# Kernel optimization log

Measured on AMD Instinct MI355X. Metric: run time of the kernel, lower is better.

Reference implementation:

```python
import jax, jax.numpy as jnp
import numpy as np

B, C_ENC, H, W = 8, 512, 96, 96
N_SAMP = 64            # num_samples in forward
N_NODES = 2 * N_SAMP   # 64 pos + 64 neg per image
D = 256                # node feature dim after head_in_ln
N_HEADS = 8
DH = D // N_HEADS
SINKHORN_ITERS = 10


def _ln(x):
    # LayerNorm(elementwise_affine=False)
    m = x.mean(-1, keepdims=True)
    v = x.var(-1, keepdims=True)
    return (x - m) / jnp.sqrt(v + 1e-5)


def setup_inputs() -> dict:
    key = jax.random.key(0)
    ks = jax.random.split(key, 12)
    std = 0.01  # matches nn.init.normal_(std=0.01) in _init_weights
    inp = {
        "feat_s": jax.random.normal(ks[0], (B, C_ENC, H, W), jnp.float32),
        "score_s": jax.random.normal(ks[1], (B, 1, H, W), jnp.float32),
        "feat_t": jax.random.normal(ks[2], (B, C_ENC, H, W), jnp.float32),
        "score_t": jax.random.normal(ks[3], (B, 1, H, W), jnp.float32),
        "head_W1": std * jax.random.normal(ks[4], (C_ENC, D), jnp.float32),
        "head_b1": jnp.zeros((D,), jnp.float32),
        "head_W2": std * jax.random.normal(ks[5], (D, D), jnp.float32),
        "head_b2": jnp.zeros((D,), jnp.float32),
        "intra_W": jax.random.normal(ks[6], (4, D, D), jnp.float32) / jnp.sqrt(jnp.float32(D)),
        "intra_b": jnp.zeros((4, D), jnp.float32),
        "cross_W": jax.random.normal(ks[7], (4, D, D), jnp.float32) / jnp.sqrt(jnp.float32(D)),
        "cross_b": jnp.zeros((4, D), jnp.float32),
        "cls_W1": std * jax.random.normal(ks[8], (D, 128), jnp.float32),
        "cls_b1": jnp.zeros((128,), jnp.float32),
        "cls_W2": std * jax.random.normal(ks[9], (128, 1), jnp.float32),
        "cls_b2": jnp.zeros((1,), jnp.float32),
        "aff_A": jax.random.normal(ks[10], (D, D), jnp.float32) / jnp.sqrt(jnp.float32(D)),
    }
    return inp


def _sample_points(feat, score):
    # torch version: boolean-mask nonzero + random gather of 64 pos / 64 neg spatial
    # locations per image. JIT-friendly deterministic equivalent: top-64 highest
    # sigmoid scores = positives, top-64 lowest = negatives.
    s = jax.nn.sigmoid(score[:, 0].reshape(B, -1))            # [B, H*W]
    _, pos_idx = jax.lax.top_k(s, N_SAMP)
    _, neg_idx = jax.lax.top_k(-s, N_SAMP)
    idx = jnp.concatenate([pos_idx, neg_idx], axis=1)         # [B, 128]
    ff = feat.reshape(B, C_ENC, -1)                           # [B, 512, H*W]
    nodes = jnp.take_along_axis(ff, idx[:, None, :], axis=2)  # [B, 512, 128]
    nodes = nodes.transpose(0, 2, 1)                          # [B, 128, 512]
    labels = jnp.concatenate(
        [jnp.ones((B, N_SAMP, 1), feat.dtype), jnp.zeros((B, N_SAMP, 1), feat.dtype)], axis=1)
    return nodes, labels


def _mha(xq, xkv, Wp, bp):
    # standard multi-head attention (MultiHeadAttentionWrapper)
    q = xq @ Wp[0] + bp[0]
    k = xkv @ Wp[1] + bp[1]
    v = xkv @ Wp[2] + bp[2]
    sh = lambda t: t.reshape(t.shape[0], t.shape[1], N_HEADS, DH)
    att = jnp.einsum("bqhd,bkhd->bhqk", sh(q), sh(k)) / jnp.sqrt(jnp.float32(DH))
    att = jax.nn.softmax(att, axis=-1)
    o = jnp.einsum("bhqk,bkhd->bqhd", att, sh(v)).reshape(xq.shape[0], xq.shape[1], D)
    return o @ Wp[3] + bp[3], att.mean(1)


def _forward(feat_s, score_s, feat_t, score_t, head_W1, head_b1, head_W2, head_b2,
             intra_W, intra_b, cross_W, cross_b, cls_W1, cls_b1, cls_W2, cls_b2, aff_A):
    n1, l1 = _sample_points(feat_s, score_s)
    n2, l2 = _sample_points(feat_t, score_t)

    # head_in_ln: Linear -> LN -> ReLU -> Linear -> LN
    head = lambda x: _ln(jax.nn.relu(_ln(x @ head_W1 + head_b1)) @ head_W2 + head_b2)
    n1, n2 = head(n1), head(n2)

    # intra-domain graph (self-attention), shared weights for both domains
    n1, _ = _mha(n1, n1, intra_W, intra_b)
    n2, _ = _mha(n2, n2, intra_W, intra_b)

    # cross-domain graph (cross-attention both directions, shared weights)
    c1, _ = _mha(n1, n2, cross_W, cross_b)
    c2, _ = _mha(n2, n1, cross_W, cross_b)
    n1, n2 = c1, c2

    # node classification loss (BCEWithLogits, mean)
    cls = lambda x: jax.nn.relu(x @ cls_W1 + cls_b1) @ cls_W2 + cls_b2
    def bce_logits(logit, lab):
        return jnp.mean(jnp.maximum(logit, 0) - logit * lab + jnp.log1p(jnp.exp(-jnp.abs(logit))))
    node_loss = bce_logits(cls(n1), l1) + bce_logits(cls(n2), l2)

    # affinity + InstanceNorm2d(1) + sinkhorn refine
    Mmat = jnp.einsum("bnd,de,bme->bnm", n1, aff_A, n2)       # [B, 128, 128]
    mu = Mmat.mean((1, 2), keepdims=True)
    var = Mmat.var((1, 2), keepdims=True)
    K = (Mmat - mu) / jnp.sqrt(var + 1e-5)
    for _ in range(SINKHORN_ITERS):  # log-space row/col normalization
        K = K - jax.nn.logsumexp(K, axis=2, keepdims=True)
        K = K - jax.nn.logsumexp(K, axis=1, keepdims=True)
    P = jnp.exp(K)

    # matching loss = BCEFocalLoss(gamma=2, alpha=0.25) vs label-agreement matrix
    gt = (l1[:, :, 0][:, :, None] == l2[:, :, 0][:, None, :]).astype(P.dtype)
    pt = jnp.clip(P, 1e-6, 1.0 - 1e-6)
    mat_loss = jnp.mean(-0.25 * (1 - pt) ** 2 * gt * jnp.log(pt)
                        - 0.75 * pt ** 2 * (1 - gt) * jnp.log(1 - pt))

    total_loss = node_loss + 10.0 * mat_loss
    return n1, total_loss


def reference(feat_s, score_s, feat_t, score_t, head_W1, head_b1, head_W2, head_b2,
              intra_W, intra_b, cross_W, cross_b, cls_W1, cls_b1, cls_W2, cls_b2, aff_A):
    return _forward(feat_s, score_s, feat_t, score_t, head_W1, head_b1, head_W2, head_b2,
                    intra_W, intra_b, cross_W, cross_b, cls_W1, cls_b1, cls_W2, cls_b2, aff_A)
```

## Files before the change

kernel.cpp:

```cpp
#include <hip/hip_runtime.h>
#include <math.h>

#define BIMG 8
#define HW 9216
#define CENC 512
#define NN 128
#define DD 256
#define NHEAD 8
#define DH 32
#define ROWS1 1024
#define ROWS2 2048
#define TAILB 520

typedef unsigned long long ull;
typedef unsigned short u16;
typedef __attribute__((ext_vector_type(4))) float f32x4;
typedef __attribute__((ext_vector_type(4))) unsigned u32x4;
typedef __attribute__((ext_vector_type(2))) unsigned u32x2;

__device__ __forceinline__ u16 f2bf(float f) {
  unsigned u = __float_as_uint(f);
  u += 0x7fffu + ((u >> 16) & 1u);
  return (u16)(u >> 16);
}
__device__ __forceinline__ float bf2f(unsigned h) { return __uint_as_float(h << 16); }
__device__ __forceinline__ unsigned pack2(float a, float b) {
  return (unsigned)f2bf(a) | ((unsigned)f2bf(b) << 16);
}
__device__ __forceinline__ void mfma_b(f32x4& acc, u32x4 a, u32x4 b) {
  asm volatile("v_mfma_f32_16x16x32_bf16 %0, %1, %2, %0" : "+v"(acc) : "v"(a), "v"(b));
}
__device__ __forceinline__ void mfma_s(f32x4& acc, u32x4 a, u32x4 b) {
  asm volatile("s_nop 1\n\tv_mfma_f32_16x16x32_bf16 %0, %1, %2, %0" : "+v"(acc) : "v"(a), "v"(b));
}

__device__ __forceinline__ ull cmpex_keep(ull k, ull o, bool keepMax) {
  return ((k > o) == keepMax) ? k : o;
}
__device__ __forceinline__ void bsort64(ull& k, int lane) {
#pragma unroll
  for (int size = 2; size <= 64; size <<= 1) {
#pragma unroll
    for (int stride = size >> 1; stride > 0; stride >>= 1) {
      ull o = __shfl_xor(k, stride);
      bool keepMax = (((lane & size) == 0) == ((lane & stride) == 0));
      k = cmpex_keep(k, o, keepMax);
    }
  }
}
__device__ __forceinline__ void bmerge64(ull& top, ull b, int lane) {
  ull rev = __shfl_xor(b, 63);
  ull m = top > rev ? top : rev;
#pragma unroll
  for (int stride = 32; stride > 0; stride >>= 1) {
    ull o = __shfl_xor(m, stride);
    m = cmpex_keep(m, o, (lane & stride) == 0);
  }
  top = m;
}
__device__ __forceinline__ ull lds_merge(ull a, ull brev, int lane) {
  ull m = a > brev ? a : brev;
#pragma unroll
  for (int stride = 32; stride > 0; stride >>= 1) {
    ull o = __shfl_xor(m, stride);
    m = cmpex_keep(m, o, (lane & stride) == 0);
  }
  return m;
}

__global__ __launch_bounds__(512) void head_kernel(const float* __restrict__ score_s,
                                                   const float* __restrict__ score_t,
                                                   int* __restrict__ idx_out,
                                                   float* __restrict__ loss_acc,
                                                   const float* __restrict__ hw1,
                                                   const float* __restrict__ hw2,
                                                   const float* __restrict__ iw,
                                                   const float* __restrict__ cw,
                                                   const float* __restrict__ aw,
                                                   const float* __restrict__ clsW1,
                                                   const float* __restrict__ intra_b,
                                                   const float* __restrict__ cross_b,
                                                   u16* __restrict__ wt,
                                                   u16* __restrict__ w1t,
                                                   u16* __restrict__ wt_f,
                                                   float* __restrict__ bfq) {
  __shared__ union {
    struct { ull sm[512]; float tile[32][33]; } a;
    struct { float Wo[32][264]; float Wc[256][40]; } b;
  } HS;
  int tid = threadIdx.x;
  if (blockIdx.x < 32) {
    int blk = blockIdx.x;
    int bi = blk >> 1, neg = blk & 1;
    int lane = tid & 63, w = tid >> 6;
    if (blk == 0 && tid < 4) loss_acc[tid] = 0.f;
    const float* sp = (bi < 8 ? score_s : score_t) + (size_t)(bi & 7) * HW;
    int q0 = w * 18;
    ull keys[18];
#pragma unroll
    for (int j = 0; j < 18; ++j) {
      float x = sp[(q0 + j) * 64 + lane];
      unsigned ub = __float_as_uint(x);
      unsigned u = (ub & 0x80000000u) ? ~ub : (ub | 0x80000000u);
      if (neg) u = ~u;
      int gi = (q0 + j) * 64 + lane;
      keys[j] = ((ull)u << 32) | (unsigned)(~gi);
    }
    ull top1 = keys[0]; bsort64(top1, lane);
    ull top2 = keys[9]; bsort64(top2, lane);
#pragma unroll
    for (int j = 1; j < 9; ++j) {
      ull k1 = keys[j], k2 = keys[9 + j];
      bsort64(k1, lane);
      bsort64(k2, lane);
      bmerge64(top1, k1, lane);
      bmerge64(top2, k2, lane);
    }
    bmerge64(top1, top2, lane);
    HS.a.sm[w * 64 + lane] = top1;
    __syncthreads();
    if (w < 4) {
      ull m = lds_merge(HS.a.sm[(2 * w) * 64 + lane],
                        HS.a.sm[(2 * w + 1) * 64 + (63 - lane)], lane);
      HS.a.sm[(2 * w) * 64 + lane] = m;
    }
    __syncthreads();
    if (w < 2) {
      ull m = lds_merge(HS.a.sm[(4 * w) * 64 + lane],
                        HS.a.sm[(4 * w + 2) * 64 + (63 - lane)], lane);
      HS.a.sm[(4 * w) * 64 + lane] = m;
    }
    __syncthreads();
    if (w == 0) {
      ull m = lds_merge(HS.a.sm[lane], HS.a.sm[4 * 64 + (63 - lane)], lane);
      idx_out[bi * NN + neg * 64 + lane] = (int)(~(unsigned)(m & 0xffffffffull));
    }
  } else if (blockIdx.x < 800) {
    int bid = blockIdx.x - 32;
    const float* src; u16* dst; int K, k0, n0;
    if (bid < 128) {
      src = hw1; dst = wt; K = 512;
      k0 = (bid >> 3) * 32; n0 = (bid & 7) * 32;
    } else {
      int id2 = bid - 128;
      int m = id2 >> 6, tt = id2 & 63;
      K = 256;
      k0 = (tt >> 3) * 32; n0 = (tt & 7) * 32;
      src = (m == 0) ? hw2 : (m < 5) ? iw + (size_t)(m - 1) * 65536
          : (m < 9) ? cw + (size_t)(m - 5) * 65536 : aw;
      dst = wt + 131072 + (size_t)m * 65536;
    }
    int r = tid >> 3, c = (tid & 7) * 4;
    if (tid < 256) {
      float4 v = *(const float4*)&src[(size_t)(k0 + r) * 256 + n0 + c];
      HS.a.tile[r][c] = v.x; HS.a.tile[r][c + 1] = v.y;
      HS.a.tile[r][c + 2] = v.z; HS.a.tile[r][c + 3] = v.w;
    }
    __syncthreads();
    if (tid < 256) {
      u32x2 o;
      o[0] = pack2(HS.a.tile[c][r], HS.a.tile[c + 1][r]);
      o[1] = pack2(HS.a.tile[c + 2][r], HS.a.tile[c + 3][r]);
      *(u32x2*)&dst[(size_t)(n0 + r) * K + k0 + c] = o;
    }
  } else if (blockIdx.x < 832) {
    int bid3 = blockIdx.x - 800;
    int k0 = (bid3 >> 2) * 32, n0 = (bid3 & 3) * 32;
    int r = tid >> 3, c = (tid & 7) * 4;
    if (tid < 256) {
      float4 v = *(const float4*)&clsW1[(size_t)(k0 + r) * 128 + n0 + c];
      HS.a.tile[r][c] = v.x; HS.a.tile[r][c + 1] = v.y;
      HS.a.tile[r][c + 2] = v.z; HS.a.tile[r][c + 3] = v.w;
    }
    __syncthreads();
    if (tid < 256) {
      u32x2 o;
      o[0] = pack2(HS.a.tile[c][r], HS.a.tile[c + 1][r]);
      o[1] = pack2(HS.a.tile[c + 2][r], HS.a.tile[c + 3][r]);
      *(u32x2*)&w1t[(size_t)(n0 + r) * 256 + k0 + c] = o;
    }
  } else {
    int bid4 = blockIdx.x - 832;
    int z = bid4 >> 6, tt = bid4 & 63;
    int k0 = (tt >> 3) * 32, n0 = (tt & 7) * 32;
    const float* Wo = iw + 3 * 65536;
    const float* Wc = cw + (size_t)z * 65536;
    for (int e = tid; e < 2048; e += 512) {
      int row = e >> 6, c4 = (e & 63) * 4;
      *(float4*)&HS.b.Wo[row][c4] = *(const float4*)&Wo[(size_t)(k0 + row) * 256 + c4];
    }
    for (int e = tid; e < 2048; e += 512) {
      int row = e >> 3, c4 = (e & 7) * 4;
      *(float4*)&HS.b.Wc[row][c4] = *(const float4*)&Wc[(size_t)row * 256 + n0 + c4];
    }
    __syncthreads();
    int k = tid >> 4, half = (tid >> 3) & 1, nb = (tid & 7) * 4;
    float a0 = 0.f, a1 = 0.f, a2 = 0.f, a3 = 0.f;
    int jb = half * 128;
#pragma unroll 8
    for (int j = 0; j < 128; ++j) {
      float wo = HS.b.Wo[k][jb + j];
      float4 wc = *(const float4*)&HS.b.Wc[jb + j][nb];
      a0 += wo * wc.x; a1 += wo * wc.y; a2 += wo * wc.z; a3 += wo * wc.w;
    }
    a0 += __shfl_xor(a0, 8); a1 += __shfl_xor(a1, 8);
    a2 += __shfl_xor(a2, 8); a3 += __shfl_xor(a3, 8);
    if (half == 0) {
      u16* dst = wt_f + (size_t)z * 65536;
      dst[(size_t)(n0 + nb + 0) * 256 + k0 + k] = f2bf(a0);
      dst[(size_t)(n0 + nb + 1) * 256 + k0 + k] = f2bf(a1);
      dst[(size_t)(n0 + nb + 2) * 256 + k0 + k] = f2bf(a2);
      dst[(size_t)(n0 + nb + 3) * 256 + k0 + k] = f2bf(a3);
    }
    if (k0 == 0 && tid < 32) {
      float b = 0.f;
      const float* bo = intra_b + 768;
      for (int j = 0; j < 256; ++j) b += bo[j] * HS.b.Wc[j][tid];
      bfq[z * 256 + n0 + tid] = b + cross_b[z * 256 + n0 + tid];
    }
  }
}

__global__ __launch_bounds__(512) void gemm1_fused(const float* __restrict__ feat_s,
                                                   const float* __restrict__ feat_t,
                                                   const int* __restrict__ idxb,
                                                   const u16* __restrict__ wt_h1,
                                                   const float* __restrict__ head_b1,
                                                   u16* __restrict__ bufA,
                                                   float* __restrict__ st1) {
  __shared__ u16 As[16][520];
  __shared__ u16 Bs[256][40];
  int t = threadIdx.x, l = t & 63, w = t >> 6;
  int m0 = blockIdx.x * 16;
#pragma unroll
  for (int row = 0; row < 16; ++row) {
    int grow = m0 + row;
    int bi = grow >> 7, n = grow & 127, b = bi & 7;
    const float* fp = (bi < 8) ? feat_s : feat_t;
    int pos = idxb[bi * NN + n];
    As[row][t] = f2bf(fp[(size_t)b * CENC * HW + (size_t)t * HW + pos]);
  }
  __syncthreads();
  f32x4 acc[2];
  acc[0] = (f32x4){0.f, 0.f, 0.f, 0.f};
  acc[1] = (f32x4){0.f, 0.f, 0.f, 0.f};
  for (int kc = 0; kc < 16; ++kc) {
#pragma unroll
    for (int i = 0; i < 2; ++i) {
      int e = t + i * 512;
      int nn2 = e >> 2, ch8 = (e & 3) * 8;
      *(u32x4*)&Bs[nn2][ch8] = *(const u32x4*)&wt_h1[(size_t)nn2 * 512 + kc * 32 + ch8];
    }
    __syncthreads();
    u32x4 af = *(const u32x4*)&As[l & 15][kc * 32 + (l >> 4) * 8];
#pragma unroll
    for (int i = 0; i < 2; ++i) {
      u32x4 bf = *(const u32x4*)&Bs[w * 32 + i * 16 + (l & 15)][(l >> 4) * 8];
      mfma_b(acc[i], af, bf);
    }
    __syncthreads();
  }
  asm volatile("s_nop 7\n\ts_nop 7" ::);
  int rbase = m0 + (l >> 4) * 4;
#pragma unroll
  for (int i = 0; i < 2; ++i) {
    int col = w * 32 + i * 16 + (l & 15);
    float bb = head_b1[col];
#pragma unroll
    for (int r = 0; r < 4; ++r) {
      int row = rbase + r;
      float o = acc[i][r] + bb;
      bufA[(size_t)row * 256 + col] = f2bf(o);
      float s = o, q = o * o;
#pragma unroll
      for (int m = 1; m < 16; m <<= 1) { s += __shfl_xor(s, m); q += __shfl_xor(q, m); }
      if ((l & 15) == 0) {
        st1[(size_t)row * 32 + w * 2 + i]      = s;
        st1[(size_t)row * 32 + 16 + w * 2 + i] = q;
      }
    }
  }
}

template<int K>
__global__ __launch_bounds__(512) void gemm_mf(const u16* __restrict__ A,
                                               const u16* __restrict__ Wt,
                                               const float* __restrict__ bias,
                                               u16* __restrict__ Cb,
                                               float* __restrict__ Cf,
                                               int ldc,
                                               const float* __restrict__ in_stats, int in_relu,
                                               float* __restrict__ out_stats) {
  constexpr int LDK = K + 8;
  constexpr int KC = K / 8;
  __shared__ u16 As[32][LDK];
  __shared__ u16 Bs[64][LDK];
  __shared__ float mS[32], rS[32];
  int n0 = blockIdx.x * 64, m0 = blockIdx.y * 32;
  int t = threadIdx.x;
  if (in_stats) {
    if (t < 32) {
      const float* sp = in_stats + (size_t)(m0 + t) * 32;
      float s = 0.f, q = 0.f;
#pragma unroll
      for (int i = 0; i < 16; ++i) { s += sp[i]; q += sp[16 + i]; }
      float mm = s * (1.f / 256.f);
      float var = q * (1.f / 256.f) - mm * mm;
      mS[t] = mm;
      rS[t] = rsqrtf(fmaxf(var, 0.f) + 1e-5f);
    }
    __syncthreads();
  }
  for (int i = t; i < 32 * KC; i += 512) {
    int row = i / KC, c8 = (i % KC) * 8;
    u32x4 av = *(const u32x4*)&A[(size_t)(m0 + row) * K + c8];
    if (in_stats) {
      float mm = mS[row], rr = rS[row];
#pragma unroll
      for (int j = 0; j < 4; ++j) {
        float f0 = (bf2f(av[j] & 0xffffu) - mm) * rr;
        float f1 = (bf2f(av[j] >> 16) - mm) * rr;
        if (in_relu) { f0 = fmaxf(f0, 0.f); f1 = fmaxf(f1, 0.f); }
        av[j] = pack2(f0, f1);
      }
    }
    *(u32x4*)&As[row][c8] = av;
  }
  for (int i = t; i < 64 * KC; i += 512) {
    int row = i / KC, c8 = (i % KC) * 8;
    *(u32x4*)&Bs[row][c8] = *(const u32x4*)&Wt[(size_t)(n0 + row) * K + c8];
  }
  __syncthreads();
  int l = t & 63, w = t >> 6;
  int wr = w >> 2, wc = w & 3;
  int fra = wr * 16 + (l & 15);
  int frk = (l >> 4) * 8;
  int fb = wc * 16 + (l & 15);
  f32x4 acc = {0.f, 0.f, 0.f, 0.f};
#pragma unroll
  for (int ks = 0; ks < K / 32; ++ks) {
    u32x4 af = *(const u32x4*)&As[fra][ks * 32 + frk];
    u32x4 bf = *(const u32x4*)&Bs[fb][ks * 32 + frk];
    mfma_b(acc, af, bf);
  }
  asm volatile("s_nop 7\n\ts_nop 7" ::);
  int col0 = n0 + wc * 16 + (l & 15);
  int rbase = m0 + wr * 16 + (l >> 4) * 4;
  float b0 = bias ? bias[col0] : 0.f;
#pragma unroll
  for (int r = 0; r < 4; ++r) {
    int row = rbase + r;
    float o0 = acc[r] + b0;
    if (Cb) Cb[(size_t)row * 256 + col0] = f2bf(o0);
    if (Cf && row < ROWS1) Cf[(size_t)row * ldc + col0] = o0;
    if (out_stats) {
      float s0 = o0, q0 = o0 * o0;
#pragma unroll
      for (int m = 1; m < 16; m <<= 1) { s0 += __shfl_xor(s0, m); q0 += __shfl_xor(q0, m); }
      if ((l & 15) == 0) {
        int slot = (n0 >> 4) + wc;
        out_stats[(size_t)row * 32 + slot]      = s0;
        out_stats[(size_t)row * 32 + 16 + slot] = q0;
      }
    }
  }
}

template<int HASLN, int SWAP>
__global__ __launch_bounds__(1024) void fattn_kernel(const u16* __restrict__ X,
                                                     const u16* __restrict__ Wt,
                                                     const float* __restrict__ bias,
                                                     const float* __restrict__ stats,
                                                     u16* __restrict__ O) {
  __shared__ u16 Qs[128][40];
  __shared__ u16 Ks[128][40];
  __shared__ u16 Vt[32][136];
  __shared__ float Sf[128][132];
  __shared__ u16 Pb[128][136];
  __shared__ float mS[128], rS[128], dn[128];
  int blk = blockIdx.x;
  int bb = blk >> 3, h = blk & 7;
  int kb = SWAP ? (bb ^ 8) : bb;
  int baseQ = bb * 128, baseKV = kb * 128;
  int t = threadIdx.x, l = t & 63, w = t >> 6;
  if (HASLN) {
    if (t < 128) {
      const float* sp = stats + (size_t)(baseQ + t) * 32;
      float s = 0.f, q = 0.f;
#pragma unroll
      for (int i = 0; i < 16; ++i) { s += sp[i]; q += sp[16 + i]; }
      float mm = s * (1.f / 256.f);
      mS[t] = mm;
      rS[t] = rsqrtf(fmaxf(q * (1.f / 256.f) - mm * mm, 0.f) + 1e-5f);
    }
    __syncthreads();
  }
  const float scale = 0.17677669529663687f;
  int mt = w >> 1, nt = w & 1;
#pragma unroll
  for (int z = 0; z < 3; ++z) {
    const u16* Xz = X + (size_t)(z == 0 ? baseQ : baseKV) * 256;
    f32x4 acc = {0.f, 0.f, 0.f, 0.f};
    int ar = mt * 16 + (l & 15);
    int bn = h * 32 + nt * 16 + (l & 15);
#pragma unroll
    for (int ks = 0; ks < 8; ++ks) {
      int ak = ks * 32 + (l >> 4) * 8;
      u32x4 af = *(const u32x4*)&Xz[(size_t)ar * 256 + ak];
      if (HASLN) {
        float mm = mS[ar], rr = rS[ar];
#pragma unroll
        for (int j = 0; j < 4; ++j) {
          float f0 = (bf2f(af[j] & 0xffffu) - mm) * rr;
          float f1 = (bf2f(af[j] >> 16) - mm) * rr;
          af[j] = pack2(f0, f1);
        }
      }
      u32x4 bf = *(const u32x4*)&Wt[(size_t)z * 65536 + (size_t)bn * 256 + ak];
      mfma_s(acc, af, bf);
    }
    asm volatile("s_nop 7\n\ts_nop 7" ::);
    float bv = bias[z * 256 + h * 32 + nt * 16 + (l & 15)];
    int cn = nt * 16 + (l & 15);
#pragma unroll
    for (int r2 = 0; r2 < 4; ++r2) {
      int rr2 = mt * 16 + (l >> 4) * 4 + r2;
      float v = acc[r2] + bv;
      if (z == 0)      Qs[rr2][cn] = f2bf(v);
      else if (z == 1) Ks[rr2][cn] = f2bf(v);
      else             Vt[cn][rr2] = f2bf(v);
    }
  }
  __syncthreads();
#pragma unroll
  for (int i = 0; i < 4; ++i) {
    int tile = w * 4 + i, mt2 = tile >> 3, nt2 = tile & 7;
    f32x4 acc = {0.f, 0.f, 0.f, 0.f};
    u32x4 af = *(const u32x4*)&Qs[mt2 * 16 + (l & 15)][(l >> 4) * 8];
    u32x4 bf = *(const u32x4*)&Ks[nt2 * 16 + (l & 15)][(l >> 4) * 8];
    mfma_s(acc, af, bf);
    asm volatile("s_nop 7\n\ts_nop 7" ::);
#pragma unroll
    for (int r2 = 0; r2 < 4; ++r2)
      Sf[mt2 * 16 + (l >> 4) * 4 + r2][nt2 * 16 + (l & 15)] = acc[r2] * scale;
  }
  __syncthreads();
  {
    int r = t >> 3, p = t & 7;
    int js = p * 16;
    float v[16];
#pragma unroll
    for (int q4 = 0; q4 < 4; ++q4) {
      float4 f = *(const float4*)&Sf[r][js + q4 * 4];
      v[q4 * 4 + 0] = f.x; v[q4 * 4 + 1] = f.y; v[q4 * 4 + 2] = f.z; v[q4 * 4 + 3] = f.w;
    }
    float mx = v[0];
#pragma unroll
    for (int j = 1; j < 16; ++j) mx = fmaxf(mx, v[j]);
    for (int m = 1; m < 8; m <<= 1) mx = fmaxf(mx, __shfl_xor(mx, m));
    float e[16];
    float den = 0.f;
#pragma unroll
    for (int j = 0; j < 16; ++j) { e[j] = __expf(v[j] - mx); den += e[j]; }
    for (int m = 1; m < 8; m <<= 1) den += __shfl_xor(den, m);
    unsigned* pw = (unsigned*)&Pb[r][js];
#pragma unroll
    for (int jp = 0; jp < 8; ++jp) pw[jp] = pack2(e[2 * jp], e[2 * jp + 1]);
    if (p == 0) dn[r] = 1.0f / den;
  }
  __syncthreads();
  {
    f32x4 acc = {0.f, 0.f, 0.f, 0.f};
#pragma unroll
    for (int ks = 0; ks < 4; ++ks) {
      u32x4 af = *(const u32x4*)&Pb[mt * 16 + (l & 15)][ks * 32 + (l >> 4) * 8];
      u32x4 bf = *(const u32x4*)&Vt[nt * 16 + (l & 15)][ks * 32 + (l >> 4) * 8];
      mfma_s(acc, af, bf);
    }
    asm volatile("s_nop 7\n\ts_nop 7" ::);
    int cn = nt * 16 + (l & 15);
#pragma unroll
    for (int r2 = 0; r2 < 4; ++r2) {
      int rr2 = mt * 16 + (l >> 4) * 4 + r2;
      O[(size_t)(baseQ + rr2) * 256 + h * 32 + cn] = f2bf(acc[r2] * dn[rr2]);
    }
  }
}

struct SkSmem {
  union { u16 tmpL[128][264]; float Km[128][133]; } u;
  float u_[NN];
  float v_[NN];
  float red[20];
};
struct ClsSmem {
  float xs[4][256];
  float part[4][128];
  float red[8];
};
union TailSmem { SkSmem sk; ClsSmem cls; };

__device__ __forceinline__ void ticket_finalize(float* acc, float* out) {
  __threadfence();
  int tk = atomicAdd((int*)acc + 3, 1);
  if (tk == TAILB - 1) {
    float a0 = atomicAdd(acc + 0, 0.0f);
    float a1 = atomicAdd(acc + 1, 0.0f);
    out[ROWS1 * DD] = a0 + 10.0f * a1;
  }
}

__global__ __launch_bounds__(1024) void tail_kernel(const u16* __restrict__ bufH,
                                                    const u16* __restrict__ wt_af,
                                                    const u16* __restrict__ w1t,
                                                    const float* __restrict__ b1,
                                                    const float* __restrict__ W2,
                                                    const float* __restrict__ b2,
                                                    float* __restrict__ acc,
                                                    float* __restrict__ out) {
  __shared__ TailSmem sm;
  int t = threadIdx.x;
  int bid = blockIdx.x;
  if (bid < 8) {
    int b = bid;
    int l = t & 63, w = t >> 6;
    int tr = w >> 1;
    const u16* c1 = bufH + (size_t)(b * 128) * 256;
    const u16* c2 = bufH + (size_t)(1024 + b * 128) * 256;
    {
      int tcB = (w & 1) * 8;
      f32x4 accA[8];
#pragma unroll
      for (int i = 0; i < 8; ++i) accA[i] = (f32x4){0.f, 0.f, 0.f, 0.f};
      for (int ks = 0; ks < 8; ++ks) {
        int kk = ks * 32 + (l >> 4) * 8;
        u32x4 af = *(const u32x4*)&c1[(size_t)(tr * 16 + (l & 15)) * 256 + kk];
#pragma unroll
        for (int i = 0; i < 8; ++i) {
          u32x4 bf = *(const u32x4*)&wt_af[(size_t)((tcB + i) * 16 + (l & 15)) * 256 + kk];
          mfma_b(accA[i], af, bf);
        }
      }
      asm volatile("s_nop 7\n\ts_nop 7" ::);
      int rb = tr * 16 + (l >> 4) * 4;
#pragma unroll
      for (int i = 0; i < 8; ++i) {
        int col = (tcB + i) * 16 + (l & 15);
#pragma unroll
        for (int r2 = 0; r2 < 4; ++r2)
          sm.sk.u.tmpL[rb + r2][col] = f2bf(accA[i][r2]);
      }
    }
    __syncthreads();
    f32x4 aB[4];
    {
      int tcB = (w & 1) * 4;
#pragma unroll
      for (int i = 0; i < 4; ++i) aB[i] = (f32x4){0.f, 0.f, 0.f, 0.f};
      for (int ks = 0; ks < 8; ++ks) {
        int kk = ks * 32 + (l >> 4) * 8;
        u32x4 a0 = *(const u32x4*)&sm.sk.u.tmpL[tr * 16 + (l & 15)][kk];
#pragma unroll
        for (int i = 0; i < 4; ++i) {
          u32x4 bf = *(const u32x4*)&c2[(size_t)((tcB + i) * 16 + (l & 15)) * 256 + kk];
          mfma_b(aB[i], a0, bf);
        }
      }
      asm volatile("s_nop 7\n\ts_nop 7" ::);
    }
    __syncthreads();
    {
      int tcB = (w & 1) * 4;
      int rb = tr * 16 + (l >> 4) * 4;
#pragma unroll
      for (int i = 0; i < 4; ++i) {
        int col = (tcB + i) * 16 + (l & 15);
#pragma unroll
        for (int r2 = 0; r2 < 4; ++r2)
          sm.sk.u.Km[rb + r2][col] = aB[i][r2];
      }
    }
    __syncthreads();
    int r = t >> 3, cg = t & 7;
    int c = t >> 3, rg = t & 7;
    float kr[16], kc[16];
    {
#pragma unroll
      for (int q4 = 0; q4 < 4; ++q4) {
        float4 f = *(const float4*)&sm.sk.u.Km[r][cg * 16 + q4 * 4];
        kr[q4 * 4 + 0] = f.x; kr[q4 * 4 + 1] = f.y; kr[q4 * 4 + 2] = f.z; kr[q4 * 4 + 3] = f.w;
      }
#pragma unroll
      for (int q = 0; q < 16; ++q)
        kc[q] = sm.sk.u.Km[rg * 16 + q][c];
    }
    float s = 0.f;
#pragma unroll
    for (int q = 0; q < 16; ++q) s += kr[q];
    for (int m = 1; m < 64; m <<= 1) s += __shfl_xor(s, m);
    if ((t & 63) == 0) sm.sk.red[t >> 6] = s;
    __syncthreads();
    if (t == 0) { float tt = 0.f; for (int i = 0; i < 16; ++i) tt += sm.sk.red[i]; sm.sk.red[16] = tt; }
    __syncthreads();
    float mu = sm.sk.red[16] * (1.0f / 16384.f);
    __syncthreads();
    float sq = 0.f;
#pragma unroll
    for (int q = 0; q < 16; ++q) { float d = kr[q] - mu; sq += d * d; }
    for (int m = 1; m < 64; m <<= 1) sq += __shfl_xor(sq, m);
    if ((t & 63) == 0) sm.sk.red[t >> 6] = sq;
    __syncthreads();
    if (t == 0) { float tt = 0.f; for (int i = 0; i < 16; ++i) tt += sm.sk.red[i]; sm.sk.red[17] = tt; }
    __syncthreads();
    float inv = 1.0f / sqrtf(sm.sk.red[17] * (1.0f / 16384.f) + 1e-5f);
#pragma unroll
    for (int q = 0; q < 16; ++q) { kr[q] = (kr[q] - mu) * inv; kc[q] = (kc[q] - mu) * inv; }
    if (t < NN) { sm.sk.u_[t] = 0.f; sm.sk.v_[t] = 0.f; }
    __syncthreads();
    for (int iter = 0; iter < 10; ++iter) {
      float tmp[16];
      {
        const float4* vp = (const float4*)(sm.sk.v_ + cg * 16);
#pragma unroll
        for (int q4 = 0; q4 < 4; ++q4) {
          float4 f = vp[q4];
          tmp[q4 * 4 + 0] = kr[q4 * 4 + 0] - f.x; tmp[q4 * 4 + 1] = kr[q4 * 4 + 1] - f.y;
          tmp[q4 * 4 + 2] = kr[q4 * 4 + 2] - f.z; tmp[q4 * 4 + 3] = kr[q4 * 4 + 3] - f.w;
        }
        float mx = tmp[0];
#pragma unroll
        for (int q = 1; q < 16; ++q) mx = fmaxf(mx, tmp[q]);
        for (int m = 1; m < 8; m <<= 1) mx = fmaxf(mx, __shfl_xor(mx, m));
        float smv = 0.f;
#pragma unroll
        for (int q = 0; q < 16; ++q) smv += __expf(tmp[q] - mx);
        for (int m = 1; m < 8; m <<= 1) smv += __shfl_xor(smv, m);
        if (cg == 0) sm.sk.u_[r] = mx + __logf(smv);
      }
      __syncthreads();
      {
        const float4* up = (const float4*)(sm.sk.u_ + rg * 16);
#pragma unroll
        for (int q4 = 0; q4 < 4; ++q4) {
          float4 f = up[q4];
          tmp[q4 * 4 + 0] = kc[q4 * 4 + 0] - f.x; tmp[q4 * 4 + 1] = kc[q4 * 4 + 1] - f.y;
          tmp[q4 * 4 + 2] = kc[q4 * 4 + 2] - f.z; tmp[q4 * 4 + 3] = kc[q4 * 4 + 3] - f.w;
        }
        float mx = tmp[0];
#pragma unroll
        for (int q = 1; q < 16; ++q) mx = fmaxf(mx, tmp[q]);
        for (int m = 1; m < 8; m <<= 1) mx = fmaxf(mx, __shfl_xor(mx, m));
        float smv = 0.f;
#pragma unroll
        for (int q = 0; q < 16; ++q) smv += __expf(tmp[q] - mx);
        for (int m = 1; m < 8; m <<= 1) smv += __shfl_xor(smv, m);
        if (rg == 0) sm.sk.v_[c] = mx + __logf(smv);
      }
      __syncthreads();
    }
    float ur = sm.sk.u_[r];
    float fsum = 0.f;
    {
      const float4* vp = (const float4*)(sm.sk.v_ + cg * 16);
#pragma unroll
      for (int q4 = 0; q4 < 4; ++q4) {
        float4 f = vp[q4];
        float vv[4] = {f.x, f.y, f.z, f.w};
#pragma unroll
        for (int j = 0; j < 4; ++j) {
          float P = __expf(kr[q4 * 4 + j] - ur - vv[j]);
          float pt = fminf(fmaxf(P, 1e-6f), 1.0f - 1e-6f);
          int col = cg * 16 + q4 * 4 + j;
          bool gt = (r < 64) == (col < 64);
          float wgt = gt ? (-0.25f * (1.f - pt) * (1.f - pt)) : (-0.75f * pt * pt);
          float lg = gt ? __logf(pt) : __logf(1.f - pt);
          fsum += wgt * lg;
        }
      }
    }
    for (int m = 1; m < 64; m <<= 1) fsum += __shfl_xor(fsum, m);
    if ((t & 63) == 0) sm.sk.red[t >> 6] = fsum;
    __syncthreads();
    if (t == 0) {
      float tt = 0.f; for (int i = 0; i < 16; ++i) tt += sm.sk.red[i];
      atomicAdd(acc + 1, tt * (1.0f / 131072.f));
      ticket_finalize(acc, out);
    }
  } else {
    int row0 = (bid - 8) * 4;
    {
      int rr = t >> 8, cc = t & 255;
      sm.cls.xs[rr][cc] = bf2f(bufH[(size_t)(row0 + rr) * 256 + cc]);
    }
    __syncthreads();
    int grp = t >> 8, col = t & 127, kh = (t >> 7) & 1;
    const u16* wp = w1t + (size_t)col * 256 + kh * 128;
    const float* xp = &sm.cls.xs[grp][kh * 128];
    float h = 0.f;
#pragma unroll
    for (int i = 0; i < 16; ++i) {
      u32x4 wv = *(const u32x4*)&wp[i * 8];
      const float* x8 = xp + i * 8;
      h += x8[0] * bf2f(wv[0] & 0xffffu) + x8[1] * bf2f(wv[0] >> 16)
         + x8[2] * bf2f(wv[1] & 0xffffu) + x8[3] * bf2f(wv[1] >> 16)
         + x8[4] * bf2f(wv[2] & 0xffffu) + x8[5] * bf2f(wv[2] >> 16)
         + x8[6] * bf2f(wv[3] & 0xffffu) + x8[7] * bf2f(wv[3] >> 16);
    }
    if (kh == 1) sm.cls.part[grp][col] = h;
    __syncthreads();
    if (kh == 0) {
      float z = h + sm.cls.part[grp][col] + b1[col];
      float p = fmaxf(z, 0.f) * W2[col];
#pragma unroll
      for (int m = 1; m < 64; m <<= 1) p += __shfl_xor(p, m);
      if ((t & 63) == 0) sm.cls.red[grp * 2 + ((t >> 6) & 1)] = p;
    }
    __syncthreads();
    if (t == 0) {
      float total = 0.f;
      float bb2 = b2[0];
#pragma unroll
      for (int g = 0; g < 4; ++g) {
        float z = sm.cls.red[2 * g] + sm.cls.red[2 * g + 1] + bb2;
        float lab = (((row0 + g) & 127) < 64) ? 1.f : 0.f;
        total += fmaxf(z, 0.f) - z * lab + log1pf(__expf(-fabsf(z)));
      }
      atomicAdd(acc, total * (1.0f / 1024.0f));
      ticket_finalize(acc, out);
    }
  }
}

extern "C" void kernel_launch(void* const* d_in, const int* in_sizes, int n_in,
                              void* d_out, int out_size, void* d_ws, size_t ws_size,
                              hipStream_t stream) {
  const float* feat_s  = (const float*)d_in[0];
  const float* score_s = (const float*)d_in[1];
  const float* feat_t  = (const float*)d_in[2];
  const float* score_t = (const float*)d_in[3];
  const float* head_W1 = (const float*)d_in[4];
  const float* head_b1 = (const float*)d_in[5];
  const float* head_W2 = (const float*)d_in[6];
  const float* head_b2 = (const float*)d_in[7];
  const float* intra_W = (const float*)d_in[8];
  const float* intra_b = (const float*)d_in[9];
  const float* cross_W = (const float*)d_in[10];
  const float* cross_b = (const float*)d_in[11];
  const float* cls_W1  = (const float*)d_in[12];
  const float* cls_b1  = (const float*)d_in[13];
  const float* cls_W2  = (const float*)d_in[14];
  const float* cls_b2  = (const float*)d_in[15];
  const float* aff_A   = (const float*)d_in[16];

  u16* bufA  = (u16*)d_ws;
  u16* bufB  = bufA + ROWS2 * DD;
  u16* bufH  = bufB + ROWS2 * DD;
  u16* attnb = bufH + ROWS2 * DD;
  u16* atto2 = attnb + ROWS2 * DD;
  u16* wt    = atto2 + ROWS2 * DD;
  u16* w1t   = wt + 786432;
  u16* wt_f  = w1t + 32768;
  float* st1 = (float*)(wt_f + 3 * 65536);
  float* st2 = st1 + ROWS2 * 32;
  float* bfq = st2 + ROWS2 * 32;
  float* acc = bfq + 768;
  int* idxb  = (int*)(acc + 8);
  float* out_f = (float*)d_out;

  u16* wt_h1 = wt;
  u16* wt_h2 = wt + 131072;
  u16* wt_in = wt_h2 + 65536;
  u16* wt_cr = wt_in + 4 * 65536;
  u16* wt_af = wt_cr + 4 * 65536;

  head_kernel<<<1024, 512, 0, stream>>>(score_s, score_t, idxb, acc,
                                        head_W1, head_W2, intra_W, cross_W, aff_A, cls_W1,
                                        intra_b, cross_b, wt, w1t, wt_f, bfq);
  gemm1_fused<<<128, 512, 0, stream>>>(feat_s, feat_t, idxb, wt_h1, head_b1, bufA, st1);

  dim3 g1(4, 64, 1);
  const float* nulf = nullptr;
  float* nulw = nullptr;

  gemm_mf<256><<<g1, 512, 0, stream>>>(bufA, wt_h2, head_b2, bufB, nulw, 0, st1, 1, st2);
  fattn_kernel<1, 0><<<128, 1024, 0, stream>>>(bufB, wt_in, intra_b, st2, attnb);
  fattn_kernel<0, 1><<<128, 1024, 0, stream>>>(attnb, wt_f, bfq, nulf, atto2);
  gemm_mf<256><<<g1, 512, 0, stream>>>(atto2, wt_cr + 3 * 65536, cross_b + 768, bufH, out_f,
                                       256, nulf, 0, nulw);
  tail_kernel<<<TAILB, 1024, 0, stream>>>(bufH, wt_af, w1t, cls_b1, cls_W2, cls_b2,
                                          acc, out_f);
}
```

Before: 207.4 us.

## Fuse second head GEMM with LayerNorm+ReLU into the gather GEMM kernel

The first head GEMM kernel now keeps its 16x256 output tile in shared memory and computes the per-row LayerNorm statistics there. It then applies normalization and ReLU and runs the second head GEMM directly, streaming W2 from global memory. This removes one kernel launch and the global round trip of the intermediate activation and its stats buffer. The cost is that the second GEMM runs on only 128 blocks with unstaged B-operand loads, and normalized values are rounded to bf16 before the MFMA.

```diff
diff --git a/kernel.cpp b/kernel.cpp
--- a/kernel.cpp
+++ b/kernel.cpp
@@ -221,15 +221,19 @@
   }
 }
 
-__global__ __launch_bounds__(512) void gemm1_fused(const float* __restrict__ feat_s,
-                                                   const float* __restrict__ feat_t,
-                                                   const int* __restrict__ idxb,
-                                                   const u16* __restrict__ wt_h1,
-                                                   const float* __restrict__ head_b1,
-                                                   u16* __restrict__ bufA,
-                                                   float* __restrict__ st1) {
+__global__ __launch_bounds__(512) void gemm12_fused(const float* __restrict__ feat_s,
+                                                    const float* __restrict__ feat_t,
+                                                    const int* __restrict__ idxb,
+                                                    const u16* __restrict__ wt_h1,
+                                                    const float* __restrict__ head_b1,
+                                                    const u16* __restrict__ wt_h2,
+                                                    const float* __restrict__ head_b2,
+                                                    u16* __restrict__ bufB,
+                                                    float* __restrict__ st2) {
   __shared__ u16 As[16][520];
+  __shared__ u16 Yb[16][264];
   __shared__ u16 Bs[256][40];
+  __shared__ float sums[16][16], sqs[16][16], mS[16], rS[16];
   int t = threadIdx.x, l = t & 63, w = t >> 6;
   int m0 = blockIdx.x * 16;
 #pragma unroll
@@ -261,22 +265,74 @@
     __syncthreads();
   }
   asm volatile("s_nop 7\n\ts_nop 7" ::);
-  int rbase = m0 + (l >> 4) * 4;
 #pragma unroll
   for (int i = 0; i < 2; ++i) {
     int col = w * 32 + i * 16 + (l & 15);
     float bb = head_b1[col];
 #pragma unroll
     for (int r = 0; r < 4; ++r) {
-      int row = rbase + r;
+      int row = (l >> 4) * 4 + r;
       float o = acc[i][r] + bb;
-      bufA[(size_t)row * 256 + col] = f2bf(o);
+      Yb[row][col] = f2bf(o);
       float s = o, q = o * o;
 #pragma unroll
       for (int m = 1; m < 16; m <<= 1) { s += __shfl_xor(s, m); q += __shfl_xor(q, m); }
       if ((l & 15) == 0) {
-        st1[(size_t)row * 32 + w * 2 + i]      = s;
-        st1[(size_t)row * 32 + 16 + w * 2 + i] = q;
+        sums[row][w * 2 + i] = s;
+        sqs[row][w * 2 + i]  = q;
+      }
+    }
+  }
+  __syncthreads();
+  if (t < 16) {
+    float s = 0.f, q = 0.f;
+#pragma unroll
+    for (int i = 0; i < 16; ++i) { s += sums[t][i]; q += sqs[t][i]; }
+    float mm = s * (1.f / 256.f);
+    mS[t] = mm;
+    rS[t] = rsqrtf(fmaxf(q * (1.f / 256.f) - mm * mm, 0.f) + 1e-5f);
+  }
+  __syncthreads();
+  {
+    int row = t >> 5, c8 = (t & 31) * 8;
+    u32x4 v = *(const u32x4*)&Yb[row][c8];
+    float mm = mS[row], rr = rS[row];
+#pragma unroll
+    for (int j = 0; j < 4; ++j) {
+      float f0 = fmaxf((bf2f(v[j] & 0xffffu) - mm) * rr, 0.f);
+      float f1 = fmaxf((bf2f(v[j] >> 16) - mm) * rr, 0.f);
+      v[j] = pack2(f0, f1);
+    }
+    __syncthreads();
+    *(u32x4*)&Yb[row][c8] = v;
+  }
+  __syncthreads();
+#pragma unroll
+  for (int i = 0; i < 2; ++i) {
+    int n0 = (w * 2 + i) * 16;
+    f32x4 a2 = {0.f, 0.f, 0.f, 0.f};
+    int ar = l & 15;
+    int bn = n0 + (l & 15);
+#pragma unroll
+    for (int ks = 0; ks < 8; ++ks) {
+      int ak = ks * 32 + (l >> 4) * 8;
+      u32x4 af = *(const u32x4*)&Yb[ar][ak];
+      u32x4 bf = *(const u32x4*)&wt_h2[(size_t)bn * 256 + ak];
+      mfma_b(a2, af, bf);
+    }
+    asm volatile("s_nop 7\n\ts_nop 7" ::);
+    float bb = head_b2[n0 + (l & 15)];
+#pragma unroll
+    for (int r = 0; r < 4; ++r) {
+      int row = m0 + (l >> 4) * 4 + r;
+      float o = a2[r] + bb;
+      bufB[(size_t)row * 256 + n0 + (l & 15)] = f2bf(o);
+      float s = o, q = o * o;
+#pragma unroll
+      for (int m = 1; m < 16; m <<= 1) { s += __shfl_xor(s, m); q += __shfl_xor(q, m); }
+      if ((l & 15) == 0) {
+        st2[(size_t)row * 32 + w * 2 + i]      = s;
+        st2[(size_t)row * 32 + 16 + w * 2 + i] = q;
       }
     }
   }
@@ -752,16 +808,14 @@
   const float* cls_b2  = (const float*)d_in[15];
   const float* aff_A   = (const float*)d_in[16];
 
-  u16* bufA  = (u16*)d_ws;
-  u16* bufB  = bufA + ROWS2 * DD;
+  u16* bufB  = (u16*)d_ws;
   u16* bufH  = bufB + ROWS2 * DD;
   u16* attnb = bufH + ROWS2 * DD;
   u16* atto2 = attnb + ROWS2 * DD;
   u16* wt    = atto2 + ROWS2 * DD;
   u16* w1t   = wt + 786432;
   u16* wt_f  = w1t + 32768;
-  float* st1 = (float*)(wt_f + 3 * 65536);
-  float* st2 = st1 + ROWS2 * 32;
+  float* st2 = (float*)(wt_f + 3 * 65536);
   float* bfq = st2 + ROWS2 * 32;
   float* acc = bfq + 768;
   int* idxb  = (int*)(acc + 8);
@@ -776,13 +830,13 @@
   head_kernel<<<1024, 512, 0, stream>>>(score_s, score_t, idxb, acc,
                                         head_W1, head_W2, intra_W, cross_W, aff_A, cls_W1,
                                         intra_b, cross_b, wt, w1t, wt_f, bfq);
-  gemm1_fused<<<128, 512, 0, stream>>>(feat_s, feat_t, idxb, wt_h1, head_b1, bufA, st1);
+  gemm12_fused<<<128, 512, 0, stream>>>(feat_s, feat_t, idxb, wt_h1, head_b1,
+                                        wt_h2, head_b2, bufB, st2);
 
   dim3 g1(4, 64, 1);
   const float* nulf = nullptr;
   float* nulw = nullptr;
 
-  gemm_mf<256><<<g1, 512, 0, stream>>>(bufA, wt_h2, head_b2, bufB, nulw, 0, st1, 1, st2);
   fattn_kernel<1, 0><<<128, 1024, 0, stream>>>(bufB, wt_in, intra_b, st2, attnb);
   fattn_kernel<0, 1><<<128, 1024, 0, stream>>>(attnb, wt_f, bfq, nulf, atto2);
   gemm_mf<256><<<g1, 512, 0, stream>>>(atto2, wt_cr + 3 * 65536, cross_b + 768, bufH, out_f,
```

Measured after the change: 207.8 us. No clear change (+0.2%).
